# Optimization experiments

Measured on AMD Instinct MI355X. Metric: run time of the kernel, lower is better.

Reference implementation:

```python
import jax, jax.numpy as jnp
import numpy as np

FEATURE_DIM = 1024
B, N = 8, 2048


def setup_inputs() -> dict:
    key = jax.random.key(0)
    ks = jax.random.split(key, 7)
    s = 1.0 / np.sqrt(FEATURE_DIM)
    x = jax.random.normal(ks[0], (B, N, FEATURE_DIM), dtype=jnp.float32)
    Wk = jax.random.uniform(ks[1], (FEATURE_DIM, FEATURE_DIM), jnp.float32, -s, s)
    bk = jax.random.uniform(ks[2], (FEATURE_DIM,), jnp.float32, -s, s)
    Wq = jax.random.uniform(ks[3], (FEATURE_DIM, FEATURE_DIM), jnp.float32, -s, s)
    bq = jax.random.uniform(ks[4], (FEATURE_DIM,), jnp.float32, -s, s)
    Wv = jax.random.uniform(ks[5], (FEATURE_DIM, FEATURE_DIM), jnp.float32, -s, s)
    bv = jax.random.uniform(ks[6], (FEATURE_DIM,), jnp.float32, -s, s)
    return {"x": x, "Wq": Wq, "bq": bq, "Wk": Wk, "bk": bk, "Wv": Wv, "bv": bv}


def reference(x, Wq, bq, Wk, bk, Wv, bv):
    # Linear layers: y = x @ W.T + b (torch nn.Linear convention)
    q = jnp.einsum('bnd,ed->bne', x, Wq) + bq
    k = jnp.einsum('bnd,ed->bne', x, Wk) + bk
    v = jnp.einsum('bnd,ed->bne', x, Wv) + bv
    scale = jnp.sqrt(jnp.asarray(float(FEATURE_DIM), dtype=x.dtype))
    scores = jnp.einsum('bqd,bkd->bqk', q, k) / scale  # [B, N, N]
    weights = jax.nn.softmax(scores, axis=-1)
    attended = jnp.einsum('bqk,bkd->bqd', weights, v)
    return attended
```

## Files before the change

### kernel.cpp

```cpp
#include <hip/hip_runtime.h>
#include <cstdint>

typedef unsigned short u16;
typedef unsigned short u16x8 __attribute__((ext_vector_type(8)));
typedef __bf16 bf16x8 __attribute__((ext_vector_type(8)));
typedef float f32x4 __attribute__((ext_vector_type(4)));

#define CS 136
#define SMEM_BYTES (128 * CS * 2)

__device__ __forceinline__ u16 f2bf(float f) {
  uint32_t u = __float_as_uint(f);
  u += 0x7fffu + ((u >> 16) & 1u);
  return (u16)(u >> 16);
}
__device__ __forceinline__ float bf2f(u16 b) {
  return __uint_as_float(((uint32_t)b) << 16);
}

__device__ __forceinline__ void async_copy16(const void* g, void* l) {
  auto gp = reinterpret_cast<const __attribute__((address_space(1))) char*>(
      reinterpret_cast<uintptr_t>(g));
  auto lp = reinterpret_cast<__attribute__((address_space(3))) char*>(
      static_cast<uint32_t>(reinterpret_cast<uintptr_t>(l)));
  __builtin_amdgcn_global_load_lds(gp, lp, 16, 0, 0);
}

__device__ __forceinline__ void kloop64(const u16* __restrict__ gA,
                                        const u16* __restrict__ gB, char* smem,
                                        f32x4 (&acc)[4][4], int K, int lda,
                                        int ldb) {
  u16* As = (u16*)smem;
  u16* Bs = As + 128 * 64;
  const int t = threadIdx.x;
  const int w = t >> 6, l = t & 63;
  const int lm = l & 15, lq = l >> 4;
  const int wm = (w & 1) * 64, wn = (w >> 1) * 64;
  const int srow = l >> 3;
  const int schunk = (l & 7) ^ (srow & 7);
  char* AsB = smem;
  char* BsB = smem + 128 * 64 * 2;

  for (int kk = 0; kk < K; kk += 64) {
#pragma unroll
    for (int i = 0; i < 4; i++) {
      const int r = w * 8 + i * 32 + srow;
      async_copy16(gA + (long)r * lda + kk + schunk * 8,
                   AsB + w * 1024 + i * 4096);
      async_copy16(gB + (long)r * ldb + kk + schunk * 8,
                   BsB + w * 1024 + i * 4096);
    }
    __syncthreads();
    bf16x8 a0[4], a1[4], b0[4], b1[4];
#pragma unroll
    for (int i = 0; i < 4; i++) {
      const int R = wm + i * 16 + lm, rx = R & 7;
      a0[i] = *(const bf16x8*)(As + R * 64 + ((lq ^ rx) * 8));
      a1[i] = *(const bf16x8*)(As + R * 64 + (((4 + lq) ^ rx) * 8));
    }
#pragma unroll
    for (int i = 0; i < 4; i++) {
      const int R = wn + i * 16 + lm, rx = R & 7;
      b0[i] = *(const bf16x8*)(Bs + R * 64 + ((lq ^ rx) * 8));
      b1[i] = *(const bf16x8*)(Bs + R * 64 + (((4 + lq) ^ rx) * 8));
    }
#pragma unroll
    for (int i = 0; i < 4; i++)
#pragma unroll
      for (int j = 0; j < 4; j++)
        acc[i][j] = __builtin_amdgcn_mfma_f32_16x16x32_bf16(a0[i], b0[j],
                                                            acc[i][j], 0, 0, 0);
#pragma unroll
    for (int i = 0; i < 4; i++)
#pragma unroll
      for (int j = 0; j < 4; j++)
        acc[i][j] = __builtin_amdgcn_mfma_f32_16x16x32_bf16(a1[i], b1[j],
                                                            acc[i][j], 0, 0, 0);
    __syncthreads();
  }
}

__device__ __forceinline__ void epi_store_bf16(char* smem, f32x4 (&acc)[4][4],
                                               u16* __restrict__ Cp, int ldc) {
  const int t = threadIdx.x, w = t >> 6, l = t & 63;
  const int lm = l & 15, lq = l >> 4;
  const int wm = (w & 1) * 64, wn = (w >> 1) * 64;
  u16* Cs = (u16*)smem;
#pragma unroll
  for (int j = 0; j < 4; j++)
#pragma unroll
    for (int i = 0; i < 4; i++)
#pragma unroll
      for (int r = 0; r < 4; r++)
        Cs[(wm + i * 16 + lq * 4 + r) * CS + wn + j * 16 + lm] =
            f2bf(acc[i][j][r]);
  __syncthreads();
  const int rl = l >> 4, cc = l & 15;
#pragma unroll
  for (int it = 0; it < 8; it++) {
    const int row = w * 32 + it * 4 + rl;
    u16x8 v = *(const u16x8*)(Cs + row * CS + cc * 8);
    *(u16x8*)(Cp + (long)row * ldc + cc * 8) = v;
  }
}

__device__ __forceinline__ void epi_store_f32(f32x4 (&acc)[4][4],
                                              float* __restrict__ Cf, int ldc) {
  const int t = threadIdx.x, w = t >> 6, l = t & 63;
  const int lm = l & 15, lq = l >> 4;
  const int wm = (w & 1) * 64, wn = (w >> 1) * 64;
  const int gm0 = wm + lq * 4, gn0 = wn + lm;
#pragma unroll
  for (int i = 0; i < 4; i++)
#pragma unroll
    for (int j = 0; j < 4; j++)
#pragma unroll
      for (int r = 0; r < 4; r++)
        Cf[(long)(gm0 + i * 16 + r) * ldc + gn0 + j * 16] = acc[i][j][r];
}

__device__ __forceinline__ void qkv_epilogue(
    char* smem, f32x4 (&acc)[4][4], int bx, int by, u16* __restrict__ qb,
    u16* __restrict__ kb, u16* __restrict__ vt, const float* __restrict__ bq,
    const float* __restrict__ bk, const float* __restrict__ bv) {
  const int t = threadIdx.x, w = t >> 6, l = t & 63;
  const int lm = l & 15, lq = l >> 4;
  const int wm = (w & 1) * 64, wn = (w >> 1) * 64;
  const int sec = bx >> 3;
  const int nl = (bx & 7) * 128;
  const float* bias = (sec == 0) ? bq : (sec == 1) ? bk : bv;
  u16* Cs = (u16*)smem;
  const int rl = l >> 4, cc = l & 15;
  if (sec < 2) {
#pragma unroll
    for (int j = 0; j < 4; j++) {
      const float bj = bias[nl + wn + j * 16 + lm];
#pragma unroll
      for (int i = 0; i < 4; i++)
#pragma unroll
        for (int r = 0; r < 4; r++)
          Cs[(wm + i * 16 + lq * 4 + r) * CS + wn + j * 16 + lm] =
              f2bf(acc[i][j][r] + bj);
    }
    __syncthreads();
    u16* Cp = ((sec == 0) ? qb : kb) + (long)by * 128 * 1024 + nl;
#pragma unroll
    for (int it = 0; it < 8; it++) {
      const int row = w * 32 + it * 4 + rl;
      u16x8 v = *(const u16x8*)(Cs + row * CS + cc * 8);
      *(u16x8*)(Cp + (long)row * 1024 + cc * 8) = v;
    }
  } else {
#pragma unroll
    for (int j = 0; j < 4; j++) {
      const int n = wn + j * 16 + lm;
      const float bj = bias[nl + n];
#pragma unroll
      for (int i = 0; i < 4; i++) {
        const int m = wm + i * 16 + lq * 4;
        *(ushort4*)(Cs + n * CS + m) =
            make_ushort4(f2bf(acc[i][j][0] + bj), f2bf(acc[i][j][1] + bj),
                         f2bf(acc[i][j][2] + bj), f2bf(acc[i][j][3] + bj));
      }
    }
    __syncthreads();
    const int m0 = by * 128;
    const int b = m0 >> 11, ml = m0 & 2047;
    u16* Vp = vt + ((long)b * 1024 + nl) * 2048 + ml;
#pragma unroll
    for (int it = 0; it < 8; it++) {
      const int row = w * 32 + it * 4 + rl;
      u16x8 v = *(const u16x8*)(Cs + row * CS + cc * 8);
      *(u16x8*)(Vp + (long)row * 2048 + cc * 8) = v;
    }
  }
}

__device__ __forceinline__ void convert_chunk(const float* x, const float* Wq,
                                              const float* Wk, const float* Wv,
                                              u16* xb, u16* Wb, int c) {
  const float* src;
  u16* dst;
  int off;
  if (c < 4194304) {
    src = x; dst = xb; off = c;
  } else {
    int j = c - 4194304;
    int sel = j >> 18;
    off = j & 262143;
    src = (sel == 0) ? Wq : (sel == 1) ? Wk : Wv;
    dst = Wb + (long)sel * 1048576;
  }
  float4 f = ((const float4*)src)[off];
  ((ushort4*)dst)[off] = make_ushort4(f2bf(f.x), f2bf(f.y), f2bf(f.z),
                                      f2bf(f.w));
}

__global__ __launch_bounds__(256) void k_convert(const float* x,
                                                 const float* Wq,
                                                 const float* Wk,
                                                 const float* Wv, u16* xb,
                                                 u16* Wb, float* rs) {
  const int c = blockIdx.x * 256 + threadIdx.x;
  if (c < 4980736) {
    convert_chunk(x, Wq, Wk, Wv, xb, Wb, c);
  } else if (rs) {
    ((float4*)rs)[c - 4980736] = make_float4(0.f, 0.f, 0.f, 0.f);
  }
}

__global__ __launch_bounds__(256) void k_qkv(const u16* xb, const u16* Wb,
                                             u16* qb, u16* kb, u16* vt,
                                             const float* bq, const float* bk,
                                             const float* bv) {
  __shared__ __align__(16) char smem[SMEM_BYTES];
  const int bid = blockIdx.x;
  const int xcd = bid & 7, lid = bid >> 3;
  const int by = xcd * 16 + (lid & 15);
  const int bx = lid >> 4;
  f32x4 acc[4][4] = {};
  kloop64(xb + (long)by * 128 * 1024, Wb + (long)bx * 128 * 1024, smem, acc,
          1024, 1024, 1024);
  qkv_epilogue(smem, acc, bx, by, qb, kb, vt, bq, bk, bv);
}

template <int ATOM>
__global__ __launch_bounds__(256) void k_gemm_s(const u16* qb, const u16* kb,
                                                u16* S, float* rowsum) {
  __shared__ __align__(16) char smem[SMEM_BYTES];
  const int bid = blockIdx.x;
  const int xcd = bid & 7, lid = bid >> 3;
  const int z = lid >> 5, s = lid & 31;
  const int m = (xcd & 1) * 8 + (s & 7);
  const int n = (xcd >> 1) * 4 + (s >> 3);
  f32x4 acc[4][4] = {};
  kloop64(qb + (long)z * 2048 * 1024 + (long)m * 128 * 1024,
          kb + (long)z * 2048 * 1024 + (long)n * 128 * 1024, smem, acc, 1024,
          1024, 1024);
#pragma unroll
  for (int i = 0; i < 4; i++)
#pragma unroll
    for (int j = 0; j < 4; j++)
#pragma unroll
      for (int r = 0; r < 4; r++)
        acc[i][j][r] = __expf(acc[i][j][r] * 0.03125f);
  if (ATOM) {
    const int t = threadIdx.x, w = t >> 6, l = t & 63;
    const int lm = l & 15, lq = l >> 4;
    const int wm = (w & 1) * 64;
#pragma unroll
    for (int i = 0; i < 4; i++)
#pragma unroll
      for (int r = 0; r < 4; r++) {
        float p = acc[i][0][r] + acc[i][1][r] + acc[i][2][r] + acc[i][3][r];
        p += __shfl_xor(p, 1);
        p += __shfl_xor(p, 2);
        p += __shfl_xor(p, 4);
        p += __shfl_xor(p, 8);
        if (lm == 0)
          atomicAdd(&rowsum[z * 2048 + m * 128 + wm + lq * 4 + i * 16 + r], p);
      }
  }
  epi_store_bf16(smem, acc,
                 S + (long)z * 2048 * 2048 + (long)m * 128 * 2048 + n * 128,
                 2048);
}

__global__ __launch_bounds__(256) void k_rowsum(const u16* S, float* rowsum) {
  __shared__ float red[4];
  const long row = blockIdx.x;
  const int t = threadIdx.x, w = t >> 6, l = t & 63;
  uint4 raw = ((const uint4*)(S + row * 2048))[t];
  float s = bf2f((u16)(raw.x & 0xffff)) + bf2f((u16)(raw.x >> 16)) +
            bf2f((u16)(raw.y & 0xffff)) + bf2f((u16)(raw.y >> 16)) +
            bf2f((u16)(raw.z & 0xffff)) + bf2f((u16)(raw.z >> 16)) +
            bf2f((u16)(raw.w & 0xffff)) + bf2f((u16)(raw.w >> 16));
#pragma unroll
  for (int o = 32; o; o >>= 1) s += __shfl_xor(s, o);
  if (l == 0) red[w] = s;
  __syncthreads();
  if (t == 0) rowsum[row] = red[0] + red[1] + red[2] + red[3];
}

__global__ __launch_bounds__(256) void k_pv(const u16* S, const u16* vt,
                                            const float* rowsum, u16* Obf,
                                            float* outf, int direct_out) {
  __shared__ __align__(16) char smem[SMEM_BYTES];
  const int bid = blockIdx.x;
  const int xcd = bid & 7, lid = bid >> 3;
  const int z = lid >> 4, s = lid & 15;
  const int m = (xcd & 3) * 4 + (s & 3);
  const int n = (xcd >> 2) * 4 + (s >> 2);
  f32x4 acc[4][4] = {};
  kloop64(S + (long)z * 2048 * 2048 + (long)m * 128 * 2048,
          vt + (long)z * 1024 * 2048 + (long)n * 128 * 2048, smem, acc, 2048,
          2048, 2048);
  const int t = threadIdx.x, w = t >> 6, l = t & 63;
  const int lq = (l & 63) >> 4;
  const int wm = (w & 1) * 64;
#pragma unroll
  for (int i = 0; i < 4; i++)
#pragma unroll
    for (int r = 0; r < 4; r++) {
      const float inv =
          1.0f / rowsum[z * 2048 + m * 128 + wm + lq * 4 + i * 16 + r];
#pragma unroll
      for (int j = 0; j < 4; j++) acc[i][j][r] *= inv;
    }
  if (direct_out)
    epi_store_f32(acc, outf + (long)z * 2048 * 1024 + (long)m * 128 * 1024 +
                           n * 128,
                  1024);
  else
    epi_store_bf16(smem, acc,
                   Obf + (long)z * 2048 * 1024 + (long)m * 128 * 1024 +
                       n * 128,
                   1024);
}

__global__ __launch_bounds__(256) void k_expand(const u16* in, float* out) {
  int i = blockIdx.x * 256 + threadIdx.x;
  if (i >= 4194304) return;
  ushort4 u = ((const ushort4*)in)[i];
  ((float4*)out)[i] = make_float4(bf2f(u.x), bf2f(u.y), bf2f(u.z), bf2f(u.w));
}

extern "C" void kernel_launch(void* const* d_in, const int* in_sizes, int n_in,
                              void* d_out, int out_size, void* d_ws,
                              size_t ws_size, hipStream_t stream) {
  const float* x = (const float*)d_in[0];
  const float* Wq = (const float*)d_in[1];
  const float* bq = (const float*)d_in[2];
  const float* Wk = (const float*)d_in[3];
  const float* bk = (const float*)d_in[4];
  const float* Wv = (const float*)d_in[5];
  const float* bv = (const float*)d_in[6];

  const long MN = 16384L * 1024;
  u16* slot0 = (u16*)d_ws;
  u16* slot1 = slot0 + MN;
  u16* slot2 = slot1 + MN;
  u16* slot3 = slot2 + MN;
  u16* xb = (u16*)d_out;
  u16* Wb = xb + MN;

  const int bigws =
      ws_size >= (size_t)(5 * MN) * sizeof(u16) + 65536 ? 1 : 0;
  u16* S = bigws ? slot3 : (u16*)d_out;
  float* rowsum = bigws ? (float*)(slot3 + 8L * 2048 * 2048)
                        : (float*)slot0;
  u16* Obf = slot0 + 32768;
  float* outf = (float*)d_out;

  dim3 blk(256);
  k_convert<<<dim3(19472), blk, 0, stream>>>(x, Wq, Wk, Wv, xb, Wb,
                                             bigws ? rowsum : nullptr);
  k_qkv<<<dim3(3072), blk, 0, stream>>>(xb, Wb, slot0, slot1, slot2, bq, bk,
                                        bv);
  if (bigws) {
    k_gemm_s<1><<<dim3(2048), blk, 0, stream>>>(slot0, slot1, S, rowsum);
    k_pv<<<dim3(1024), blk, 0, stream>>>(S, slot2, rowsum, nullptr, outf, 1);
  } else {
    k_gemm_s<0><<<dim3(2048), blk, 0, stream>>>(slot0, slot1, S, nullptr);
    k_rowsum<<<dim3(16384), blk, 0, stream>>>(S, rowsum);
    k_pv<<<dim3(1024), blk, 0, stream>>>(S, slot2, rowsum, Obf, nullptr, 0);
    k_expand<<<dim3(16384), blk, 0, stream>>>(Obf, outf);
  }
}
```

Before: 430.3 us.

## Move all three GEMMs to 256x256 tiles with 8-wave double-buffered LDS pipeline

Replaces the 128x128, 4-wave single-stage GEMM loop with a 256x256 tile per 512-thread block. Two K-stages are double-buffered in 128KB of LDS, and global-to-LDS async loads are interleaved with MFMA phases. Explicit vmcnt waits, barriers and s_setprio keep the matrix cores busy while the next tiles stream in. The Q/K/V projection, score and PV kernels and their epilogues are rewritten for the larger tile. This cuts global/LDS traffic per FLOP and exposes more latency hiding, at the cost of much larger register and LDS footprint, one block per CU, and fewer blocks than CUs to fill in some kernels.

```diff
diff --git a/kernel.cpp b/kernel.cpp
--- a/kernel.cpp
+++ b/kernel.cpp
@@ -6,8 +6,8 @@
 typedef __bf16 bf16x8 __attribute__((ext_vector_type(8)));
 typedef float f32x4 __attribute__((ext_vector_type(4)));
 
-#define CS 136
-#define SMEM_BYTES (128 * CS * 2)
+#define CS2 264
+#define SMEM256 131072
 
 __device__ __forceinline__ u16 f2bf(float f) {
   uint32_t u = __float_as_uint(f);
@@ -26,153 +26,160 @@
   __builtin_amdgcn_global_load_lds(gp, lp, 16, 0, 0);
 }
 
-__device__ __forceinline__ void kloop64(const u16* __restrict__ gA,
-                                        const u16* __restrict__ gB, char* smem,
-                                        f32x4 (&acc)[4][4], int K, int lda,
-                                        int ldb) {
-  u16* As = (u16*)smem;
-  u16* Bs = As + 128 * 64;
+__device__ __forceinline__ void barrier_() {
+  asm volatile("" ::: "memory");
+  __builtin_amdgcn_s_barrier();
+  asm volatile("" ::: "memory");
+}
+#define LGKM0() asm volatile("s_waitcnt lgkmcnt(0)" ::: "memory")
+#define VMC(N) asm volatile("s_waitcnt vmcnt(" #N ")" ::: "memory")
+
+template <int NT, int LDA, int LDB>
+__device__ __forceinline__ void gemm256(const u16* __restrict__ gA,
+                                        const u16* __restrict__ gB, char* lds,
+                                        f32x4 (&acc)[8][4]) {
   const int t = threadIdx.x;
   const int w = t >> 6, l = t & 63;
   const int lm = l & 15, lq = l >> 4;
-  const int wm = (w & 1) * 64, wn = (w >> 1) * 64;
-  const int srow = l >> 3;
-  const int schunk = (l & 7) ^ (srow & 7);
-  char* AsB = smem;
-  char* BsB = smem + 128 * 64 * 2;
-
-  for (int kk = 0; kk < K; kk += 64) {
-#pragma unroll
-    for (int i = 0; i < 4; i++) {
-      const int r = w * 8 + i * 32 + srow;
-      async_copy16(gA + (long)r * lda + kk + schunk * 8,
-                   AsB + w * 1024 + i * 4096);
-      async_copy16(gB + (long)r * ldb + kk + schunk * 8,
-                   BsB + w * 1024 + i * 4096);
-    }
-    __syncthreads();
-    bf16x8 a0[4], a1[4], b0[4], b1[4];
-#pragma unroll
-    for (int i = 0; i < 4; i++) {
-      const int R = wm + i * 16 + lm, rx = R & 7;
-      a0[i] = *(const bf16x8*)(As + R * 64 + ((lq ^ rx) * 8));
-      a1[i] = *(const bf16x8*)(As + R * 64 + (((4 + lq) ^ rx) * 8));
-    }
-#pragma unroll
-    for (int i = 0; i < 4; i++) {
-      const int R = wn + i * 16 + lm, rx = R & 7;
-      b0[i] = *(const bf16x8*)(Bs + R * 64 + ((lq ^ rx) * 8));
-      b1[i] = *(const bf16x8*)(Bs + R * 64 + (((4 + lq) ^ rx) * 8));
-    }
-#pragma unroll
-    for (int i = 0; i < 4; i++)
-#pragma unroll
-      for (int j = 0; j < 4; j++)
-        acc[i][j] = __builtin_amdgcn_mfma_f32_16x16x32_bf16(a0[i], b0[j],
-                                                            acc[i][j], 0, 0, 0);
-#pragma unroll
-    for (int i = 0; i < 4; i++)
-#pragma unroll
-      for (int j = 0; j < 4; j++)
-        acc[i][j] = __builtin_amdgcn_mfma_f32_16x16x32_bf16(a1[i], b1[j],
-                                                            acc[i][j], 0, 0, 0);
-    __syncthreads();
-  }
-}
-
-__device__ __forceinline__ void epi_store_bf16(char* smem, f32x4 (&acc)[4][4],
-                                               u16* __restrict__ Cp, int ldc) {
+  const int wr = w & 1, wc = w >> 1;
+
+  const u16* gAt = gA + (long)(t >> 3) * LDA + ((t & 7) ^ ((t >> 3) & 7)) * 8;
+  const u16* gBt = gB + (long)(t >> 3) * LDB + ((t & 7) ^ ((t >> 3) & 7)) * 8;
+  char* ldsw = lds + w * 1024;
+
+  bf16x8 a[8], b0[4], b1[4];
+
+  auto stA = [&](int P, int h, int kt) {
+#pragma unroll
+    for (int s = 0; s < 2; s++)
+      async_copy16(gAt + (long)(h * 128 + s * 64) * LDA + kt * 64,
+                   ldsw + P * 65536 + h * 16384 + s * 8192);
+  };
+  auto stB = [&](int P, int h, int kt) {
+#pragma unroll
+    for (int s = 0; s < 2; s++)
+      async_copy16(gBt + (long)(h * 128 + s * 64) * LDB + kt * 64,
+                   ldsw + P * 65536 + 32768 + h * 16384 + s * 8192);
+  };
+  auto rdA = [&](int P, int h) {
+#pragma unroll
+    for (int il = 0; il < 4; il++) {
+      const int r = wr * 64 + il * 16 + lm;
+      const char* base = lds + P * 65536 + h * 16384 + r * 128;
+#pragma unroll
+      for (int ks = 0; ks < 2; ks++)
+        a[il * 2 + ks] = *(const bf16x8*)(base + ((ks * 4 + lq) ^ (r & 7)) * 16);
+    }
+  };
+  auto rdB = [&](bf16x8(&b)[4], int P, int h) {
+#pragma unroll
+    for (int jl = 0; jl < 2; jl++) {
+      const int r = wc * 32 + jl * 16 + lm;
+      const char* base = lds + P * 65536 + 32768 + h * 16384 + r * 128;
+#pragma unroll
+      for (int ks = 0; ks < 2; ks++)
+        b[jl * 2 + ks] = *(const bf16x8*)(base + ((ks * 4 + lq) ^ (r & 7)) * 16);
+    }
+  };
+  auto mma = [&](int mh, int nh, const bf16x8(&b)[4]) {
+    __builtin_amdgcn_s_setprio(1);
+#pragma unroll
+    for (int il = 0; il < 4; il++)
+#pragma unroll
+      for (int jl = 0; jl < 2; jl++)
+#pragma unroll
+        for (int ks = 0; ks < 2; ks++)
+          acc[mh * 4 + il][nh * 2 + jl] =
+              __builtin_amdgcn_mfma_f32_16x16x32_bf16(
+                  a[il * 2 + ks], b[jl * 2 + ks], acc[mh * 4 + il][nh * 2 + jl],
+                  0, 0, 0);
+    __builtin_amdgcn_s_setprio(0);
+  };
+
+  stA(0, 0, 0); stB(0, 0, 0); stB(0, 1, 0); stA(0, 1, 0);
+  stA(1, 0, 1); stB(1, 0, 1); stB(1, 1, 1);
+  VMC(6);
+  barrier_();
+
+#pragma unroll 1
+  for (int i = 0; i < NT / 2 - 1; ++i) {
+    const int kt = 2 * i;
+    rdA(0, 0); rdB(b0, 0, 0);
+    stA(1, 1, kt + 1);
+    barrier_(); LGKM0(); mma(0, 0, b0); barrier_();
+    rdB(b1, 0, 1);
+    stA(0, 0, kt + 2);
+    barrier_(); LGKM0(); mma(0, 1, b1); barrier_();
+    rdA(0, 1);
+    stB(0, 0, kt + 2);
+    barrier_(); LGKM0(); mma(1, 0, b0); barrier_();
+    stB(0, 1, kt + 2);
+    barrier_(); mma(1, 1, b1);
+    VMC(6);
+    barrier_();
+    rdA(1, 0); rdB(b0, 1, 0);
+    stA(0, 1, kt + 2);
+    barrier_(); LGKM0(); mma(0, 0, b0); barrier_();
+    rdB(b1, 1, 1);
+    stA(1, 0, kt + 3);
+    barrier_(); LGKM0(); mma(0, 1, b1); barrier_();
+    rdA(1, 1);
+    stB(1, 0, kt + 3);
+    barrier_(); LGKM0(); mma(1, 0, b0); barrier_();
+    stB(1, 1, kt + 3);
+    barrier_(); mma(1, 1, b1);
+    VMC(6);
+    barrier_();
+  }
+  rdA(0, 0); rdB(b0, 0, 0);
+  stA(1, 1, NT - 1);
+  barrier_(); LGKM0(); mma(0, 0, b0); barrier_();
+  rdB(b1, 0, 1);
+  barrier_(); LGKM0(); mma(0, 1, b1); barrier_();
+  rdA(0, 1);
+  barrier_(); LGKM0(); mma(1, 0, b0); barrier_();
+  barrier_(); mma(1, 1, b1);
+  VMC(0);
+  barrier_();
+  rdA(1, 0); rdB(b0, 1, 0);
+  barrier_(); LGKM0(); mma(0, 0, b0); barrier_();
+  rdB(b1, 1, 1);
+  barrier_(); LGKM0(); mma(0, 1, b1); barrier_();
+  rdA(1, 1);
+  barrier_(); LGKM0(); mma(1, 0, b0); barrier_();
+  mma(1, 1, b1);
+  barrier_();
+}
+
+__device__ __forceinline__ void epi256_bf16(char* lds, f32x4 (&acc)[8][4],
+                                            u16* __restrict__ Cp, int ldc,
+                                            const float* __restrict__ bias) {
   const int t = threadIdx.x, w = t >> 6, l = t & 63;
   const int lm = l & 15, lq = l >> 4;
-  const int wm = (w & 1) * 64, wn = (w >> 1) * 64;
-  u16* Cs = (u16*)smem;
-#pragma unroll
-  for (int j = 0; j < 4; j++)
-#pragma unroll
-    for (int i = 0; i < 4; i++)
-#pragma unroll
-      for (int r = 0; r < 4; r++)
-        Cs[(wm + i * 16 + lq * 4 + r) * CS + wn + j * 16 + lm] =
-            f2bf(acc[i][j][r]);
-  __syncthreads();
-  const int rl = l >> 4, cc = l & 15;
-#pragma unroll
-  for (int it = 0; it < 8; it++) {
-    const int row = w * 32 + it * 4 + rl;
-    u16x8 v = *(const u16x8*)(Cs + row * CS + cc * 8);
-    *(u16x8*)(Cp + (long)row * ldc + cc * 8) = v;
-  }
-}
-
-__device__ __forceinline__ void epi_store_f32(f32x4 (&acc)[4][4],
-                                              float* __restrict__ Cf, int ldc) {
-  const int t = threadIdx.x, w = t >> 6, l = t & 63;
-  const int lm = l & 15, lq = l >> 4;
-  const int wm = (w & 1) * 64, wn = (w >> 1) * 64;
-  const int gm0 = wm + lq * 4, gn0 = wn + lm;
-#pragma unroll
-  for (int i = 0; i < 4; i++)
-#pragma unroll
-    for (int j = 0; j < 4; j++)
-#pragma unroll
-      for (int r = 0; r < 4; r++)
-        Cf[(long)(gm0 + i * 16 + r) * ldc + gn0 + j * 16] = acc[i][j][r];
-}
-
-__device__ __forceinline__ void qkv_epilogue(
-    char* smem, f32x4 (&acc)[4][4], int bx, int by, u16* __restrict__ qb,
-    u16* __restrict__ kb, u16* __restrict__ vt, const float* __restrict__ bq,
-    const float* __restrict__ bk, const float* __restrict__ bv) {
-  const int t = threadIdx.x, w = t >> 6, l = t & 63;
-  const int lm = l & 15, lq = l >> 4;
-  const int wm = (w & 1) * 64, wn = (w >> 1) * 64;
-  const int sec = bx >> 3;
-  const int nl = (bx & 7) * 128;
-  const float* bias = (sec == 0) ? bq : (sec == 1) ? bk : bv;
-  u16* Cs = (u16*)smem;
-  const int rl = l >> 4, cc = l & 15;
-  if (sec < 2) {
+  const int wr = w & 1, wc = w >> 1;
+  u16* Cs = (u16*)lds;
+#pragma unroll
+  for (int mh = 0; mh < 2; mh++) {
 #pragma unroll
     for (int j = 0; j < 4; j++) {
-      const float bj = bias[nl + wn + j * 16 + lm];
-#pragma unroll
-      for (int i = 0; i < 4; i++)
+      const int ncol = (j >> 1) * 128 + wc * 32 + (j & 1) * 16 + lm;
+      const float bj = bias ? bias[ncol] : 0.f;
+#pragma unroll
+      for (int il = 0; il < 4; il++) {
+        const int rrow = wr * 64 + il * 16 + lq * 4;
 #pragma unroll
         for (int r = 0; r < 4; r++)
-          Cs[(wm + i * 16 + lq * 4 + r) * CS + wn + j * 16 + lm] =
-              f2bf(acc[i][j][r] + bj);
+          Cs[(rrow + r) * CS2 + ncol] = f2bf(acc[mh * 4 + il][j][r] + bj);
+      }
     }
     __syncthreads();
-    u16* Cp = ((sec == 0) ? qb : kb) + (long)by * 128 * 1024 + nl;
 #pragma unroll
     for (int it = 0; it < 8; it++) {
-      const int row = w * 32 + it * 4 + rl;
-      u16x8 v = *(const u16x8*)(Cs + row * CS + cc * 8);
-      *(u16x8*)(Cp + (long)row * 1024 + cc * 8) = v;
-    }
-  } else {
-#pragma unroll
-    for (int j = 0; j < 4; j++) {
-      const int n = wn + j * 16 + lm;
-      const float bj = bias[nl + n];
-#pragma unroll
-      for (int i = 0; i < 4; i++) {
-        const int m = wm + i * 16 + lq * 4;
-        *(ushort4*)(Cs + n * CS + m) =
-            make_ushort4(f2bf(acc[i][j][0] + bj), f2bf(acc[i][j][1] + bj),
-                         f2bf(acc[i][j][2] + bj), f2bf(acc[i][j][3] + bj));
-      }
+      const int row = it * 16 + (t >> 5);
+      u16x8 v = *(const u16x8*)(Cs + row * CS2 + (t & 31) * 8);
+      *(u16x8*)(Cp + (long)(mh * 128 + row) * ldc + (t & 31) * 8) = v;
     }
     __syncthreads();
-    const int m0 = by * 128;
-    const int b = m0 >> 11, ml = m0 & 2047;
-    u16* Vp = vt + ((long)b * 1024 + nl) * 2048 + ml;
-#pragma unroll
-    for (int it = 0; it < 8; it++) {
-      const int row = w * 32 + it * 4 + rl;
-      u16x8 v = *(const u16x8*)(Cs + row * CS + cc * 8);
-      *(u16x8*)(Vp + (long)row * 2048 + cc * 8) = v;
-    }
   }
 }
 
@@ -209,47 +216,82 @@
   }
 }
 
-__global__ __launch_bounds__(256) void k_qkv(const u16* xb, const u16* Wb,
-                                             u16* qb, u16* kb, u16* vt,
-                                             const float* bq, const float* bk,
-                                             const float* bv) {
-  __shared__ __align__(16) char smem[SMEM_BYTES];
+__global__ __launch_bounds__(512, 2) void k_qkv256(
+    const u16* xb, const u16* Wb, u16* qb, u16* kb, u16* vt,
+    const float* bq, const float* bk, const float* bv) {
+  __shared__ __align__(16) char lds[SMEM256];
   const int bid = blockIdx.x;
   const int xcd = bid & 7, lid = bid >> 3;
-  const int by = xcd * 16 + (lid & 15);
-  const int bx = lid >> 4;
-  f32x4 acc[4][4] = {};
-  kloop64(xb + (long)by * 128 * 1024, Wb + (long)bx * 128 * 1024, smem, acc,
-          1024, 1024, 1024);
-  qkv_epilogue(smem, acc, bx, by, qb, kb, vt, bq, bk, bv);
-}
-
-template <int ATOM>
-__global__ __launch_bounds__(256) void k_gemm_s(const u16* qb, const u16* kb,
-                                                u16* S, float* rowsum) {
-  __shared__ __align__(16) char smem[SMEM_BYTES];
+  const int by = xcd * 8 + (lid & 7);
+  const int bx = lid >> 3;
+  f32x4 acc[8][4] = {};
+  gemm256<16, 1024, 1024>(xb + (long)by * 256 * 1024,
+                          Wb + (long)bx * 256 * 1024, lds, acc);
+  const int t = threadIdx.x, w = t >> 6, l = t & 63;
+  const int lm = l & 15, lq = l >> 4;
+  const int wr = w & 1, wc = w >> 1;
+  const int sec = bx >> 2;
+  const int nl = (bx & 3) * 256;
+  const float* bias = (sec == 0) ? bq : (sec == 1) ? bk : bv;
+  u16* Cs = (u16*)lds;
+  if (sec < 2) {
+    u16* Cp = ((sec == 0) ? qb : kb) + (long)by * 256 * 1024 + nl;
+    epi256_bf16(lds, acc, Cp, 1024, bias + nl);
+  } else {
+    const int m0 = by * 256, b = m0 >> 11, ml = m0 & 2047;
+#pragma unroll
+    for (int nh = 0; nh < 2; nh++) {
+#pragma unroll
+      for (int jl = 0; jl < 2; jl++) {
+        const int j = nh * 2 + jl;
+        const int nloc = wc * 32 + jl * 16 + lm;
+        const float bj = bias[nl + nh * 128 + nloc];
+#pragma unroll
+        for (int i = 0; i < 8; i++) {
+          const int mloc = (i >> 2) * 128 + wr * 64 + (i & 3) * 16 + lq * 4;
+          *(ushort4*)(Cs + nloc * CS2 + mloc) =
+              make_ushort4(f2bf(acc[i][j][0] + bj), f2bf(acc[i][j][1] + bj),
+                           f2bf(acc[i][j][2] + bj), f2bf(acc[i][j][3] + bj));
+        }
+      }
+      __syncthreads();
+      u16* Vp = vt + ((long)b * 1024 + nl + nh * 128) * 2048 + ml;
+#pragma unroll
+      for (int it = 0; it < 8; it++) {
+        const int nrow = it * 16 + (t >> 5);
+        u16x8 v = *(const u16x8*)(Cs + nrow * CS2 + (t & 31) * 8);
+        *(u16x8*)(Vp + (long)nrow * 2048 + (t & 31) * 8) = v;
+      }
+      __syncthreads();
+    }
+  }
+}
+
+__global__ __launch_bounds__(512, 2) void k_s256(const u16* qb, const u16* kb,
+                                                 u16* S, float* rowsum) {
+  __shared__ __align__(16) char lds[SMEM256];
   const int bid = blockIdx.x;
   const int xcd = bid & 7, lid = bid >> 3;
-  const int z = lid >> 5, s = lid & 31;
-  const int m = (xcd & 1) * 8 + (s & 7);
-  const int n = (xcd >> 1) * 4 + (s >> 3);
-  f32x4 acc[4][4] = {};
-  kloop64(qb + (long)z * 2048 * 1024 + (long)m * 128 * 1024,
-          kb + (long)z * 2048 * 1024 + (long)n * 128 * 1024, smem, acc, 1024,
-          1024, 1024);
-#pragma unroll
-  for (int i = 0; i < 4; i++)
+  const int z = lid >> 3, s = lid & 7;
+  const int m = (xcd & 1) * 4 + (s & 3);
+  const int n = (xcd >> 1) * 2 + (s >> 2);
+  f32x4 acc[8][4] = {};
+  gemm256<16, 1024, 1024>(qb + (long)z * 2048 * 1024 + (long)m * 256 * 1024,
+                          kb + (long)z * 2048 * 1024 + (long)n * 256 * 1024,
+                          lds, acc);
+  const int t = threadIdx.x, w = t >> 6, l = t & 63;
+  const int lm = l & 15, lq = l >> 4;
+  const int wr = w & 1;
+#pragma unroll
+  for (int i = 0; i < 8; i++)
 #pragma unroll
     for (int j = 0; j < 4; j++)
 #pragma unroll
       for (int r = 0; r < 4; r++)
         acc[i][j][r] = __expf(acc[i][j][r] * 0.03125f);
-  if (ATOM) {
-    const int t = threadIdx.x, w = t >> 6, l = t & 63;
-    const int lm = l & 15, lq = l >> 4;
-    const int wm = (w & 1) * 64;
-#pragma unroll
-    for (int i = 0; i < 4; i++)
+  if (rowsum) {
+#pragma unroll
+    for (int i = 0; i < 8; i++)
 #pragma unroll
       for (int r = 0; r < 4; r++) {
         float p = acc[i][0][r] + acc[i][1][r] + acc[i][2][r] + acc[i][3][r];
@@ -258,12 +300,14 @@
         p += __shfl_xor(p, 4);
         p += __shfl_xor(p, 8);
         if (lm == 0)
-          atomicAdd(&rowsum[z * 2048 + m * 128 + wm + lq * 4 + i * 16 + r], p);
+          atomicAdd(&rowsum[z * 2048 + m * 256 + (i >> 2) * 128 + wr * 64 +
+                            (i & 3) * 16 + lq * 4 + r],
+                    p);
       }
   }
-  epi_store_bf16(smem, acc,
-                 S + (long)z * 2048 * 2048 + (long)m * 128 * 2048 + n * 128,
-                 2048);
+  epi256_bf16(lds, acc,
+              S + (long)z * 2048 * 2048 + (long)m * 256 * 2048 + n * 256, 2048,
+              nullptr);
 }
 
 __global__ __launch_bounds__(256) void k_rowsum(const u16* S, float* rowsum) {
@@ -282,40 +326,50 @@
   if (t == 0) rowsum[row] = red[0] + red[1] + red[2] + red[3];
 }
 
-__global__ __launch_bounds__(256) void k_pv(const u16* S, const u16* vt,
-                                            const float* rowsum, u16* Obf,
-                                            float* outf, int direct_out) {
-  __shared__ __align__(16) char smem[SMEM_BYTES];
+__global__ __launch_bounds__(512, 2) void k_pv256(const u16* S, const u16* vt,
+                                                  const float* rowsum,
+                                                  u16* Obf, float* outf,
+                                                  int direct_out) {
+  __shared__ __align__(16) char lds[SMEM256];
   const int bid = blockIdx.x;
   const int xcd = bid & 7, lid = bid >> 3;
-  const int z = lid >> 4, s = lid & 15;
-  const int m = (xcd & 3) * 4 + (s & 3);
-  const int n = (xcd >> 2) * 4 + (s >> 2);
-  f32x4 acc[4][4] = {};
-  kloop64(S + (long)z * 2048 * 2048 + (long)m * 128 * 2048,
-          vt + (long)z * 1024 * 2048 + (long)n * 128 * 2048, smem, acc, 2048,
-          2048, 2048);
+  const int z = lid >> 2, s = lid & 3;
+  const int m = (xcd & 3) * 2 + (s & 1);
+  const int n = (xcd >> 2) * 2 + (s >> 1);
+  f32x4 acc[8][4] = {};
+  gemm256<32, 2048, 2048>(S + (long)z * 2048 * 2048 + (long)m * 256 * 2048,
+                          vt + (long)z * 1024 * 2048 + (long)n * 256 * 2048,
+                          lds, acc);
   const int t = threadIdx.x, w = t >> 6, l = t & 63;
-  const int lq = (l & 63) >> 4;
-  const int wm = (w & 1) * 64;
-#pragma unroll
-  for (int i = 0; i < 4; i++)
+  const int lm = l & 15, lq = l >> 4;
+  const int wr = w & 1, wc = w >> 1;
+#pragma unroll
+  for (int i = 0; i < 8; i++)
 #pragma unroll
     for (int r = 0; r < 4; r++) {
-      const float inv =
-          1.0f / rowsum[z * 2048 + m * 128 + wm + lq * 4 + i * 16 + r];
+      const float inv = 1.0f / rowsum[z * 2048 + m * 256 + (i >> 2) * 128 +
+                                      wr * 64 + (i & 3) * 16 + lq * 4 + r];
 #pragma unroll
       for (int j = 0; j < 4; j++) acc[i][j][r] *= inv;
     }
-  if (direct_out)
-    epi_store_f32(acc, outf + (long)z * 2048 * 1024 + (long)m * 128 * 1024 +
-                           n * 128,
-                  1024);
-  else
-    epi_store_bf16(smem, acc,
-                   Obf + (long)z * 2048 * 1024 + (long)m * 128 * 1024 +
-                       n * 128,
-                   1024);
+  if (direct_out) {
+    float* Cf = outf + (long)z * 2048 * 1024 + (long)m * 256 * 1024 + n * 256;
+#pragma unroll
+    for (int i = 0; i < 8; i++) {
+      const int gm = (i >> 2) * 128 + wr * 64 + (i & 3) * 16 + lq * 4;
+#pragma unroll
+      for (int j = 0; j < 4; j++) {
+        const int gn = (j >> 1) * 128 + wc * 32 + (j & 1) * 16 + lm;
+#pragma unroll
+        for (int r = 0; r < 4; r++)
+          Cf[(long)(gm + r) * 1024 + gn] = acc[i][j][r];
+      }
+    }
+  } else {
+    epi256_bf16(lds, acc,
+                Obf + (long)z * 2048 * 1024 + (long)m * 256 * 1024 + n * 256,
+                1024, nullptr);
+  }
 }
 
 __global__ __launch_bounds__(256) void k_expand(const u16* in, float* out) {
@@ -352,18 +406,20 @@
   u16* Obf = slot0 + 32768;
   float* outf = (float*)d_out;
 
-  dim3 blk(256);
+  dim3 blk(256), blk5(512);
   k_convert<<<dim3(19472), blk, 0, stream>>>(x, Wq, Wk, Wv, xb, Wb,
                                              bigws ? rowsum : nullptr);
-  k_qkv<<<dim3(3072), blk, 0, stream>>>(xb, Wb, slot0, slot1, slot2, bq, bk,
-                                        bv);
+  k_qkv256<<<dim3(768), blk5, 0, stream>>>(xb, Wb, slot0, slot1, slot2, bq,
+                                           bk, bv);
   if (bigws) {
-    k_gemm_s<1><<<dim3(2048), blk, 0, stream>>>(slot0, slot1, S, rowsum);
-    k_pv<<<dim3(1024), blk, 0, stream>>>(S, slot2, rowsum, nullptr, outf, 1);
+    k_s256<<<dim3(512), blk5, 0, stream>>>(slot0, slot1, S, rowsum);
+    k_pv256<<<dim3(256), blk5, 0, stream>>>(S, slot2, rowsum, nullptr, outf,
+                                            1);
   } else {
-    k_gemm_s<0><<<dim3(2048), blk, 0, stream>>>(slot0, slot1, S, nullptr);
+    k_s256<<<dim3(512), blk5, 0, stream>>>(slot0, slot1, S, nullptr);
     k_rowsum<<<dim3(16384), blk, 0, stream>>>(S, rowsum);
-    k_pv<<<dim3(1024), blk, 0, stream>>>(S, slot2, rowsum, Obf, nullptr, 0);
+    k_pv256<<<dim3(256), blk5, 0, stream>>>(S, slot2, rowsum, Obf, nullptr,
+                                            0);
     k_expand<<<dim3(16384), blk, 0, stream>>>(Obf, outf);
   }
 }
```

New measurement: 349.0 us. 18.9% less time.
